# Kernel tuning notes

Measured on AMD Instinct MI355X. Metric: run time of the kernel, lower is better.

Reference implementation:

```python
import jax, jax.numpy as jnp
import numpy as np

E, H, I = 8, 1024, 512          # experts, hidden, moe_intermediate
NG, TKG, TOPK = 4, 2, 4          # n_group, topk_group, num_experts_per_tok
SCALE = 2.5                      # routed_scaling_factor


def _mlp(x, wg, wu, wd):
    # SwiGLU MLP: down(silu(gate(x)) * up(x)), all bias-free
    return (jax.nn.silu(x @ wg) * (x @ wu)) @ wd


def setup_inputs() -> dict:
    key = jax.random.key(0)
    ks = jax.random.split(key, 8)
    s = 0.02
    return {
        "hidden_states": jax.random.normal(ks[0], (32, 256, H), jnp.float32),
        "gate_w": jax.random.normal(ks[1], (E, H), jnp.float32) * np.float32(np.sqrt(2.0 / H)),
        "correction_bias": jnp.zeros((E,), jnp.float32),
        "Wg": jax.random.normal(ks[2], (E, H, I), jnp.float32) * s,
        "Wu": jax.random.normal(ks[3], (E, H, I), jnp.float32) * s,
        "Wd": jax.random.normal(ks[4], (E, I, H), jnp.float32) * s,
        "Wg_s": jax.random.normal(ks[5], (H, I), jnp.float32) * s,
        "Wu_s": jax.random.normal(ks[6], (H, I), jnp.float32) * s,
        "Wd_s": jax.random.normal(ks[7], (I, H), jnp.float32) * s,
    }


def reference(hidden_states, gate_w, correction_bias, Wg, Wu, Wd, Wg_s, Wu_s, Wd_s):
    B, T, _ = hidden_states.shape
    x = hidden_states.reshape(-1, H)                     # [N, H]
    N = x.shape[0]

    # ---- TopkRouter + route_tokens_to_experts (float32 router math) ----
    logits = x @ gate_w.T                                # [N, E]
    scores = jax.nn.sigmoid(logits)
    scores_c = scores + correction_bias                  # scores for choice
    grp = scores_c.reshape(N, NG, E // NG)
    group_scores = jnp.sum(jax.lax.top_k(grp, 2)[0], axis=-1)        # [N, NG]
    grp_idx = jax.lax.top_k(group_scores, TKG)[1]                    # [N, TKG]
    group_mask = jnp.zeros_like(group_scores).at[
        jnp.arange(N)[:, None], grp_idx].set(1.0)                    # [N, NG]
    score_mask = jnp.repeat(group_mask, E // NG, axis=-1) > 0.5      # [N, E]
    scores_for_choice = jnp.where(score_mask, scores_c, 0.0)
    topk_idx = jax.lax.top_k(scores_for_choice, TOPK)[1]             # [N, K]
    topk_w = jnp.take_along_axis(scores, topk_idx, axis=-1)          # [N, K]
    topk_w = topk_w / (jnp.sum(topk_w, axis=-1, keepdims=True) + 1e-20)
    topk_w = topk_w * SCALE

    # ---- DSNaiveMoE: equivalent dense-expert combine ----
    # combine weight per (token, expert); zero for unrouted pairs, so the
    # dense evaluation produces exactly the gather/scatter loop's result.
    cw = jnp.sum(jax.nn.one_hot(topk_idx, E, dtype=topk_w.dtype) * topk_w[..., None], axis=1)  # [N, E]
    g = jnp.einsum('nh,ehi->eni', x, Wg)
    u = jnp.einsum('nh,ehi->eni', x, Wu)
    y = jnp.einsum('eni,eih->enh', jax.nn.silu(g) * u, Wd)           # [E, N, H]
    routed = jnp.einsum('enh,ne->nh', y, cw)                          # [N, H]

    # ---- shared expert on residual input (replaces residual add) ----
    out = routed + _mlp(x, Wg_s, Wu_s, Wd_s)
    return out.reshape(B, T, H)
```

## Files before the change

### kernel.cpp

```cpp
#include <hip/hip_runtime.h>

#define E_ 8
#define H_ 1024
#define I_ 512
#define NE 9
#define NTOK 8192
#define NROWS 40960

typedef __bf16 bf16;
typedef __bf16 bf16x8 __attribute__((ext_vector_type(8)));
typedef __bf16 bf16x4 __attribute__((ext_vector_type(4)));
typedef float f32x4 __attribute__((ext_vector_type(4)));

__device__ __forceinline__ void gload16(const bf16* g, bf16* l) {
  __builtin_amdgcn_global_load_lds(
      (const __attribute__((address_space(1))) void*)g,
      (__attribute__((address_space(3))) void*)l,
      16, 0, 0);
}

#define PREP_CONV 2048
#define PREP_TRANS 3456
__global__ __launch_bounds__(256) void prep_kernel(
    const float* __restrict__ x, const float* __restrict__ gw,
    const float* __restrict__ bias,
    const float* __restrict__ Wg, const float* __restrict__ Wu,
    const float* __restrict__ Wd, const float* __restrict__ Wgs,
    const float* __restrict__ Wus, const float* __restrict__ Wds,
    bf16* __restrict__ xb, bf16* __restrict__ BgT, bf16* __restrict__ BuT,
    bf16* __restrict__ WdT, int4* __restrict__ topk_e, float4* __restrict__ topk_w) {
  __shared__ bf16 tile[64][66];
  int bid = blockIdx.x;
  int t = threadIdx.x;

  if (bid < PREP_CONV) {
    size_t base = (size_t)bid * 1024 + t;
#pragma unroll
    for (int j = 0; j < 4; j++) {
      f32x4 v = ((const f32x4*)x)[base + 256 * j];
      bf16x4 o = {(bf16)v.x, (bf16)v.y, (bf16)v.z, (bf16)v.w};
      ((bf16x4*)xb)[base + 256 * j] = o;
    }
    return;
  }
  if (bid < PREP_CONV + PREP_TRANS) {
    int b = bid - PREP_CONV;
    int job = b >> 7;
    int tl = b & 127;
    const float* src;
    bf16* dst;
    int C, dst_ld, tr, tc;
    if (job < 18) {
      int e = job % 9;
      if (job < 9) src = (e < 8) ? Wg + (size_t)e * H_ * I_ : Wgs;
      else         src = (e < 8) ? Wu + (size_t)e * H_ * I_ : Wus;
      dst = ((job < 9) ? BgT : BuT) + (size_t)e * I_ * H_;
      C = I_; dst_ld = H_;
      tr = tl >> 3; tc = tl & 7;
    } else {
      int e = job - 18;
      src = (e < 8) ? Wd + (size_t)e * I_ * H_ : Wds;
      dst = WdT + (size_t)e * H_ * I_;
      C = H_; dst_ld = I_;
      tr = tl >> 4; tc = tl & 15;
    }
    int lx = t & 63, ly = t >> 6;
#pragma unroll
    for (int j = 0; j < 16; j++) {
      int rl = j * 4 + ly;
      tile[lx][rl] = (bf16)src[(size_t)(tr * 64 + rl) * C + tc * 64 + lx];
    }
    __syncthreads();
#pragma unroll
    for (int j = 0; j < 16; j++) {
      int cl = j * 4 + ly;
      dst[(size_t)(tc * 64 + cl) * dst_ld + tr * 64 + lx] = tile[cl][lx];
    }
    return;
  }
  int rb = bid - PREP_CONV - PREP_TRANS;
  int l = t & 63, w = t >> 6;
  int n = rb * 4 + w;
  const f32x4* xr = (const f32x4*)(x + (size_t)n * H_ + l * 16);
  float xv[16];
#pragma unroll
  for (int q = 0; q < 4; q++) {
    f32x4 v = xr[q];
    xv[q * 4 + 0] = v.x; xv[q * 4 + 1] = v.y; xv[q * 4 + 2] = v.z; xv[q * 4 + 3] = v.w;
  }
  float acc[E_];
#pragma unroll
  for (int e = 0; e < E_; e++) {
    const f32x4* gr = (const f32x4*)(gw + e * H_ + l * 16);
    float a = 0.f;
#pragma unroll
    for (int q = 0; q < 4; q++) {
      f32x4 g = gr[q];
      a += xv[q * 4 + 0] * g.x + xv[q * 4 + 1] * g.y + xv[q * 4 + 2] * g.z + xv[q * 4 + 3] * g.w;
    }
    acc[e] = a;
  }
#pragma unroll
  for (int off = 32; off > 0; off >>= 1) {
    float tmp[E_];
#pragma unroll
    for (int e = 0; e < E_; e++) tmp[e] = __shfl_xor(acc[e], off, 64);
#pragma unroll
    for (int e = 0; e < E_; e++) acc[e] += tmp[e];
  }
  if (l == 0) {
    float s[E_], sc[E_];
#pragma unroll
    for (int e = 0; e < E_; e++) {
      s[e] = 1.f / (1.f + __expf(-acc[e]));
      sc[e] = s[e] + bias[e];
    }
    float gs[4];
#pragma unroll
    for (int g = 0; g < 4; g++) gs[g] = sc[2 * g] + sc[2 * g + 1];
    int g0 = 0;
    for (int g = 1; g < 4; g++) if (gs[g] > gs[g0]) g0 = g;
    int g1 = -1;
    for (int g = 0; g < 4; g++) {
      if (g == g0) continue;
      if (g1 < 0 || gs[g] > gs[g1]) g1 = g;
    }
    int es[4] = {2 * g0, 2 * g0 + 1, 2 * g1, 2 * g1 + 1};
    float wsum = 1e-20f;
    for (int j = 0; j < 4; j++) wsum += s[es[j]];
    float inv = 2.5f / wsum;
    topk_e[n] = (int4){es[0], es[1], es[2], es[3]};
    topk_w[n] = (float4){s[es[0]] * inv, s[es[1]] * inv, s[es[2]] * inv, s[es[3]] * inv};
  }
}

__global__ __launch_bounds__(256) void compact_kernel(
    const int4* __restrict__ topk_e, const float4* __restrict__ topk_w,
    int* __restrict__ cnt, int* __restrict__ idx, float* __restrict__ cwp,
    int* __restrict__ tokpos) {
  __shared__ int hist[E_];
  __shared__ int base[E_];
  int t = threadIdx.x;
  if (t < E_) hist[t] = 0;
  __syncthreads();
  int n = blockIdx.x * 256 + t;
  int4 e4 = topk_e[n];
  float4 w4 = topk_w[n];
  int le[4] = {e4.x, e4.y, e4.z, e4.w};
  float lw[4] = {w4.x, w4.y, w4.z, w4.w};
  int lpos[4];
#pragma unroll
  for (int j = 0; j < 4; j++) lpos[j] = atomicAdd(&hist[le[j]], 1);
  __syncthreads();
  if (t < E_) base[t] = atomicAdd(&cnt[t], hist[t]);
  __syncthreads();
#pragma unroll
  for (int j = 0; j < 4; j++) {
    int p = base[le[j]] + lpos[j];
    idx[le[j] * NTOK + p] = n;
    cwp[le[j] * NTOK + p] = lw[j];
    tokpos[n * 4 + j] = (le[j] << 13) | p;
  }
}

__device__ __forceinline__ bool slot_decode(const int* cnt, int slot,
                                            int& e, int& m0, int& ne, int& off_e) {
  int off = 0, s = slot;
  for (int ee = 0; ee < NE; ee++) {
    int c = (ee < E_) ? cnt[ee] : NTOK;
    int tl = (c + 127) >> 7;
    if (s < tl) { e = ee; m0 = s * 128; ne = c; off_e = off; return true; }
    s -= tl;
    off += c;
  }
  return false;
}


__global__ __launch_bounds__(256, 2) void gemm1_kernel(
    const bf16* __restrict__ X, const bf16* __restrict__ BgT,
    const bf16* __restrict__ BuT, const int* __restrict__ idx,
    const float* __restrict__ cwp, const int* __restrict__ cnt,
    bf16* __restrict__ Tc) {
  int e, m0, ne, off_e;
  if (!slot_decode(cnt, blockIdx.y, e, m0, ne, off_e)) return;

  __shared__ bf16 As[128 * 64], Bgs[128 * 64], Bus[128 * 64];
  int t = threadIdx.x;
  int l = t & 63, w = t >> 6;
  int wm = w >> 1, wn = w & 1;
  int n0 = blockIdx.x * 128;

  f32x4 accg[4][4], accu[4][4];
#pragma unroll
  for (int mi = 0; mi < 4; mi++)
#pragma unroll
    for (int ni = 0; ni < 4; ni++) {
      accg[mi][ni] = (f32x4){0.f, 0.f, 0.f, 0.f};
      accu[mi][ni] = (f32x4){0.f, 0.f, 0.f, 0.f};
    }

  int srow = t >> 3;
  int scol = (((t & 7) ^ ((t >> 3) & 7)) * 8);
  int rid[4];
#pragma unroll
  for (int i = 0; i < 4; i++) {
    int r = m0 + srow + 32 * i;
    rid[i] = (e < 8) ? ((r < ne) ? idx[e * NTOK + r] : 0) : r;
  }
  const bf16* gg = BgT + (size_t)e * I_ * H_ + (size_t)(n0 + srow) * H_ + scol;
  const bf16* gu = BuT + (size_t)e * I_ * H_ + (size_t)(n0 + srow) * H_ + scol;
  bf16* la = As + w * 512;
  bf16* lg = Bgs + w * 512;
  bf16* lu = Bus + w * 512;

  for (int k0 = 0; k0 < H_; k0 += 64) {
#pragma unroll
    for (int i = 0; i < 4; i++) {
      gload16(X + (size_t)rid[i] * H_ + scol + k0, la + i * 2048);
      gload16(gg + (size_t)i * 32 * H_ + k0, lg + i * 2048);
      gload16(gu + (size_t)i * 32 * H_ + k0, lu + i * 2048);
    }
    __syncthreads();
#pragma unroll
    for (int ks = 0; ks < 2; ks++) {
      int ko = (((ks * 4 + (l >> 4)) ^ (l & 7)) * 8);
      int ar = wm * 64 + (l & 15);
      int br = wn * 64 + (l & 15);
      bf16x8 af[4], bg[4], bu[4];
#pragma unroll
      for (int mi = 0; mi < 4; mi++)
        af[mi] = *(const bf16x8*)(As + (ar + mi * 16) * 64 + ko);
#pragma unroll
      for (int ni = 0; ni < 4; ni++) {
        bg[ni] = *(const bf16x8*)(Bgs + (br + ni * 16) * 64 + ko);
        bu[ni] = *(const bf16x8*)(Bus + (br + ni * 16) * 64 + ko);
      }
#pragma unroll
      for (int mi = 0; mi < 4; mi++)
#pragma unroll
        for (int ni = 0; ni < 4; ni++) {
          accg[mi][ni] = __builtin_amdgcn_mfma_f32_16x16x32_bf16(af[mi], bg[ni], accg[mi][ni], 0, 0, 0);
          accu[mi][ni] = __builtin_amdgcn_mfma_f32_16x16x32_bf16(af[mi], bu[ni], accu[mi][ni], 0, 0, 0);
        }
    }
    __syncthreads();
  }
#pragma unroll
  for (int mi = 0; mi < 4; mi++) {
#pragma unroll
    for (int r = 0; r < 4; r++) {
      int lr = wm * 64 + mi * 16 + (l >> 4) * 4 + r;
      int pr = m0 + lr;
      if (pr < ne) {
        float c = (e < 8) ? cwp[e * NTOK + pr] : 1.0f;
#pragma unroll
        for (int ni = 0; ni < 4; ni++) {
          float g = accg[mi][ni][r];
          float u = accu[mi][ni][r];
          float val = c * (g / (1.f + __expf(-g))) * u;
          int col = n0 + wn * 64 + ni * 16 + (l & 15);
          Tc[(size_t)(off_e + pr) * I_ + col] = (bf16)val;
        }
      }
    }
  }
}

__global__ __launch_bounds__(256, 3) void gemm2_kernel(
    const bf16* __restrict__ Tc, const bf16* __restrict__ WdT,
    const int* __restrict__ cnt, bf16* __restrict__ Yp) {
  int e, m0, ne, off_e;
  if (!slot_decode(cnt, blockIdx.y, e, m0, ne, off_e)) return;

  __shared__ bf16 As[128 * 64], Bs[128 * 64];
  int t = threadIdx.x;
  int l = t & 63, w = t >> 6;
  int wm = w >> 1, wn = w & 1;
  int n0 = blockIdx.x * 128;

  f32x4 acc[4][4];
#pragma unroll
  for (int mi = 0; mi < 4; mi++)
#pragma unroll
    for (int ni = 0; ni < 4; ni++) acc[mi][ni] = (f32x4){0.f, 0.f, 0.f, 0.f};

  int srow = t >> 3;
  int scol = (((t & 7) ^ ((t >> 3) & 7)) * 8);
  const bf16* ga = Tc + (size_t)(off_e + m0 + srow) * I_ + scol;
  const bf16* gb = WdT + (size_t)e * H_ * I_ + (size_t)(n0 + srow) * I_ + scol;
  bf16* la = As + w * 512;
  bf16* lb = Bs + w * 512;

  for (int k0 = 0; k0 < I_; k0 += 64) {
#pragma unroll
    for (int i = 0; i < 4; i++) {
      gload16(ga + (size_t)i * 32 * I_ + k0, la + i * 2048);
      gload16(gb + (size_t)i * 32 * I_ + k0, lb + i * 2048);
    }
    __syncthreads();
#pragma unroll
    for (int ks = 0; ks < 2; ks++) {
      int ko = (((ks * 4 + (l >> 4)) ^ (l & 7)) * 8);
      int ar = wm * 64 + (l & 15);
      int br = wn * 64 + (l & 15);
      bf16x8 af[4], bfv[4];
#pragma unroll
      for (int mi = 0; mi < 4; mi++)
        af[mi] = *(const bf16x8*)(As + (ar + mi * 16) * 64 + ko);
#pragma unroll
      for (int ni = 0; ni < 4; ni++)
        bfv[ni] = *(const bf16x8*)(Bs + (br + ni * 16) * 64 + ko);
#pragma unroll
      for (int mi = 0; mi < 4; mi++)
#pragma unroll
        for (int ni = 0; ni < 4; ni++)
          acc[mi][ni] = __builtin_amdgcn_mfma_f32_16x16x32_bf16(af[mi], bfv[ni], acc[mi][ni], 0, 0, 0);
    }
    __syncthreads();
  }
#pragma unroll
  for (int mi = 0; mi < 4; mi++) {
#pragma unroll
    for (int r = 0; r < 4; r++) {
      int lr = wm * 64 + mi * 16 + (l >> 4) * 4 + r;
      int pr = m0 + lr;
      if (pr < ne) {
#pragma unroll
        for (int ni = 0; ni < 4; ni++) {
          int col = n0 + wn * 64 + ni * 16 + (l & 15);
          Yp[(size_t)(off_e + pr) * H_ + col] = (bf16)acc[mi][ni][r];
        }
      }
    }
  }
}

__global__ __launch_bounds__(256) void combine_kernel(
    const int* __restrict__ cnt, const int* __restrict__ tokpos,
    const bf16* __restrict__ Yp, float* __restrict__ out) {
  int t = threadIdx.x;
  int tok = blockIdx.x * 2 + (t >> 7);
  int cb = (t & 127) * 8;
  int off[E_];
  int a = 0;
#pragma unroll
  for (int e = 0; e < E_; e++) { off[e] = a; a += cnt[e]; }
  float sum[8];
  {
    bf16x8 v = *(const bf16x8*)(Yp + (size_t)(32768 + tok) * H_ + cb);
#pragma unroll
    for (int q = 0; q < 8; q++) sum[q] = (float)v[q];
  }
#pragma unroll
  for (int j = 0; j < 4; j++) {
    int tp = tokpos[tok * 4 + j];
    int e = tp >> 13, p = tp & 8191;
    bf16x8 v = *(const bf16x8*)(Yp + (size_t)(off[e] + p) * H_ + cb);
#pragma unroll
    for (int q = 0; q < 8; q++) sum[q] += (float)v[q];
  }
  float* op = out + (size_t)tok * H_ + cb;
  *(f32x4*)(op) = (f32x4){sum[0], sum[1], sum[2], sum[3]};
  *(f32x4*)(op + 4) = (f32x4){sum[4], sum[5], sum[6], sum[7]};
}

extern "C" void kernel_launch(void* const* d_in, const int* in_sizes, int n_in,
                              void* d_out, int out_size, void* d_ws, size_t ws_size,
                              hipStream_t stream) {
  const float* x   = (const float*)d_in[0];
  const float* gw  = (const float*)d_in[1];
  const float* cb  = (const float*)d_in[2];
  const float* Wg  = (const float*)d_in[3];
  const float* Wu  = (const float*)d_in[4];
  const float* Wd  = (const float*)d_in[5];
  const float* Wgs = (const float*)d_in[6];
  const float* Wus = (const float*)d_in[7];
  const float* Wds = (const float*)d_in[8];

  char* ws = (char*)d_ws;
  size_t off = 0;
  int*    cnt    = (int*)(ws + off);    off += 64;
  int*    idx    = (int*)(ws + off);    off += (size_t)E_ * NTOK * 4;
  float*  cwp    = (float*)(ws + off);  off += (size_t)E_ * NTOK * 4;
  int4*   topk_e = (int4*)(ws + off);   off += (size_t)NTOK * 16;
  float4* topk_w = (float4*)(ws + off); off += (size_t)NTOK * 16;
  int*    tokpos = (int*)(ws + off);    off += (size_t)NTOK * 4 * 4;
  bf16* BgT = (bf16*)(ws + off);  off += (size_t)NE * I_ * H_ * 2;
  bf16* BuT = (bf16*)(ws + off);  off += (size_t)NE * I_ * H_ * 2;
  bf16* WdT = (bf16*)(ws + off);  off += (size_t)NE * H_ * I_ * 2;
  bf16* Xb  = (bf16*)(ws + off);  off += (size_t)NTOK * H_ * 2;
  bf16* Tc  = (bf16*)(ws + off);  off += (size_t)NROWS * I_ * 2;
  bf16* Yp  = (bf16*)(ws + off);  off += (size_t)NROWS * H_ * 2;

  hipMemsetAsync(cnt, 0, 64, stream);
  hipLaunchKernelGGL(prep_kernel, dim3(PREP_CONV + PREP_TRANS + NTOK / 4), dim3(256), 0, stream,
                     x, gw, cb, Wg, Wu, Wd, Wgs, Wus, Wds,
                     Xb, BgT, BuT, WdT, topk_e, topk_w);
  hipLaunchKernelGGL(compact_kernel, dim3(NTOK / 256), dim3(256), 0, stream,
                     topk_e, topk_w, cnt, idx, cwp, tokpos);
  hipLaunchKernelGGL(gemm1_kernel, dim3(4, 328), dim3(256), 0, stream,
                     Xb, BgT, BuT, idx, cwp, cnt, Tc);
  hipLaunchKernelGGL(gemm2_kernel, dim3(8, 328), dim3(256), 0, stream,
                     Tc, WdT, cnt, Yp);
  hipLaunchKernelGGL(combine_kernel, dim3(NTOK / 2), dim3(256), 0, stream,
                     cnt, tokpos, Yp, (float*)d_out);
}
```

Before: 379.4 us.

## Use persistent XCD-aware tile scheduling so each XCD handles one expert

After: 536.5 us. +41.4%, slower.

```diff
diff --git a/kernel.cpp b/kernel.cpp
--- a/kernel.cpp
+++ b/kernel.cpp
@@ -163,173 +163,187 @@
   }
 }
 
-__device__ __forceinline__ bool slot_decode(const int* cnt, int slot,
-                                            int& e, int& m0, int& ne, int& off_e) {
-  int off = 0, s = slot;
-  for (int ee = 0; ee < NE; ee++) {
-    int c = (ee < E_) ? cnt[ee] : NTOK;
-    int tl = (c + 127) >> 7;
-    if (s < tl) { e = ee; m0 = s * 128; ne = c; off_e = off; return true; }
-    s -= tl;
-    off += c;
+__device__ __forceinline__ bool xcd_decode(const int* cnt, int g, int j, int ntiles,
+                                           int& e, int& m0, int& ne, int& off_e, int& n0) {
+  int ne_g = cnt[g];
+  int Tg = ((ne_g + 127) >> 7) * ntiles;
+  if (j < Tg) {
+    e = g; ne = ne_g;
+    m0 = (j / ntiles) * 128; n0 = (j % ntiles) * 128;
+    int off = 0;
+    for (int ee = 0; ee < E_; ee++) off += (ee < g) ? cnt[ee] : 0;
+    off_e = off;
+    return true;
+  }
+  int s = (j - Tg) * 8 + g;
+  if (s < 64 * ntiles) {
+    e = 8; ne = NTOK; off_e = 4 * NTOK;
+    m0 = (s / ntiles) * 128; n0 = (s % ntiles) * 128;
+    return true;
   }
   return false;
 }
 
 
-__global__ __launch_bounds__(256, 2) void gemm1_kernel(
+__global__ __launch_bounds__(256, 3) void gemm1_kernel(
     const bf16* __restrict__ X, const bf16* __restrict__ BgT,
     const bf16* __restrict__ BuT, const int* __restrict__ idx,
     const float* __restrict__ cwp, const int* __restrict__ cnt,
     bf16* __restrict__ Tc) {
-  int e, m0, ne, off_e;
-  if (!slot_decode(cnt, blockIdx.y, e, m0, ne, off_e)) return;
-
   __shared__ bf16 As[128 * 64], Bgs[128 * 64], Bus[128 * 64];
   int t = threadIdx.x;
   int l = t & 63, w = t >> 6;
   int wm = w >> 1, wn = w & 1;
-  int n0 = blockIdx.x * 128;
-
-  f32x4 accg[4][4], accu[4][4];
-#pragma unroll
-  for (int mi = 0; mi < 4; mi++)
-#pragma unroll
-    for (int ni = 0; ni < 4; ni++) {
-      accg[mi][ni] = (f32x4){0.f, 0.f, 0.f, 0.f};
-      accu[mi][ni] = (f32x4){0.f, 0.f, 0.f, 0.f};
-    }
-
   int srow = t >> 3;
   int scol = (((t & 7) ^ ((t >> 3) & 7)) * 8);
-  int rid[4];
-#pragma unroll
-  for (int i = 0; i < 4; i++) {
-    int r = m0 + srow + 32 * i;
-    rid[i] = (e < 8) ? ((r < ne) ? idx[e * NTOK + r] : 0) : r;
-  }
-  const bf16* gg = BgT + (size_t)e * I_ * H_ + (size_t)(n0 + srow) * H_ + scol;
-  const bf16* gu = BuT + (size_t)e * I_ * H_ + (size_t)(n0 + srow) * H_ + scol;
   bf16* la = As + w * 512;
   bf16* lg = Bgs + w * 512;
   bf16* lu = Bus + w * 512;
-
-  for (int k0 = 0; k0 < H_; k0 += 64) {
+  int g = blockIdx.x & 7;
+  int S = gridDim.x >> 3;
+
+  for (int j = blockIdx.x >> 3; ; j += S) {
+    int e, m0, ne, off_e, n0;
+    if (!xcd_decode(cnt, g, j, 4, e, m0, ne, off_e, n0)) break;
+
+    f32x4 accg[4][4], accu[4][4];
+#pragma unroll
+    for (int mi = 0; mi < 4; mi++)
+#pragma unroll
+      for (int ni = 0; ni < 4; ni++) {
+        accg[mi][ni] = (f32x4){0.f, 0.f, 0.f, 0.f};
+        accu[mi][ni] = (f32x4){0.f, 0.f, 0.f, 0.f};
+      }
+
+    int rid[4];
 #pragma unroll
     for (int i = 0; i < 4; i++) {
-      gload16(X + (size_t)rid[i] * H_ + scol + k0, la + i * 2048);
-      gload16(gg + (size_t)i * 32 * H_ + k0, lg + i * 2048);
-      gload16(gu + (size_t)i * 32 * H_ + k0, lu + i * 2048);
-    }
-    __syncthreads();
-#pragma unroll
-    for (int ks = 0; ks < 2; ks++) {
-      int ko = (((ks * 4 + (l >> 4)) ^ (l & 7)) * 8);
-      int ar = wm * 64 + (l & 15);
-      int br = wn * 64 + (l & 15);
-      bf16x8 af[4], bg[4], bu[4];
-#pragma unroll
-      for (int mi = 0; mi < 4; mi++)
-        af[mi] = *(const bf16x8*)(As + (ar + mi * 16) * 64 + ko);
-#pragma unroll
-      for (int ni = 0; ni < 4; ni++) {
-        bg[ni] = *(const bf16x8*)(Bgs + (br + ni * 16) * 64 + ko);
-        bu[ni] = *(const bf16x8*)(Bus + (br + ni * 16) * 64 + ko);
-      }
-#pragma unroll
-      for (int mi = 0; mi < 4; mi++)
+      int r = m0 + srow + 32 * i;
+      rid[i] = (e < 8) ? ((r < ne) ? idx[e * NTOK + r] : 0) : r;
+    }
+    const bf16* gg = BgT + (size_t)e * I_ * H_ + (size_t)(n0 + srow) * H_ + scol;
+    const bf16* gu = BuT + (size_t)e * I_ * H_ + (size_t)(n0 + srow) * H_ + scol;
+
+    for (int k0 = 0; k0 < H_; k0 += 64) {
+#pragma unroll
+      for (int i = 0; i < 4; i++) {
+        gload16(X + (size_t)rid[i] * H_ + scol + k0, la + i * 2048);
+        gload16(gg + (size_t)i * 32 * H_ + k0, lg + i * 2048);
+        gload16(gu + (size_t)i * 32 * H_ + k0, lu + i * 2048);
+      }
+      __syncthreads();
+#pragma unroll
+      for (int ks = 0; ks < 2; ks++) {
+        int ko = (((ks * 4 + (l >> 4)) ^ (l & 7)) * 8);
+        int ar = wm * 64 + (l & 15);
+        int br = wn * 64 + (l & 15);
+        bf16x8 af[4], bg[4], bu[4];
+#pragma unroll
+        for (int mi = 0; mi < 4; mi++)
+          af[mi] = *(const bf16x8*)(As + (ar + mi * 16) * 64 + ko);
 #pragma unroll
         for (int ni = 0; ni < 4; ni++) {
-          accg[mi][ni] = __builtin_amdgcn_mfma_f32_16x16x32_bf16(af[mi], bg[ni], accg[mi][ni], 0, 0, 0);
-          accu[mi][ni] = __builtin_amdgcn_mfma_f32_16x16x32_bf16(af[mi], bu[ni], accu[mi][ni], 0, 0, 0);
+          bg[ni] = *(const bf16x8*)(Bgs + (br + ni * 16) * 64 + ko);
+          bu[ni] = *(const bf16x8*)(Bus + (br + ni * 16) * 64 + ko);
         }
-    }
-    __syncthreads();
-  }
-#pragma unroll
-  for (int mi = 0; mi < 4; mi++) {
-#pragma unroll
-    for (int r = 0; r < 4; r++) {
-      int lr = wm * 64 + mi * 16 + (l >> 4) * 4 + r;
-      int pr = m0 + lr;
-      if (pr < ne) {
-        float c = (e < 8) ? cwp[e * NTOK + pr] : 1.0f;
-#pragma unroll
-        for (int ni = 0; ni < 4; ni++) {
-          float g = accg[mi][ni][r];
-          float u = accu[mi][ni][r];
-          float val = c * (g / (1.f + __expf(-g))) * u;
-          int col = n0 + wn * 64 + ni * 16 + (l & 15);
-          Tc[(size_t)(off_e + pr) * I_ + col] = (bf16)val;
+#pragma unroll
+        for (int mi = 0; mi < 4; mi++)
+#pragma unroll
+          for (int ni = 0; ni < 4; ni++) {
+            accg[mi][ni] = __builtin_amdgcn_mfma_f32_16x16x32_bf16(af[mi], bg[ni], accg[mi][ni], 0, 0, 0);
+            accu[mi][ni] = __builtin_amdgcn_mfma_f32_16x16x32_bf16(af[mi], bu[ni], accu[mi][ni], 0, 0, 0);
+          }
+      }
+      __syncthreads();
+    }
+#pragma unroll
+    for (int mi = 0; mi < 4; mi++) {
+#pragma unroll
+      for (int r = 0; r < 4; r++) {
+        int lr = wm * 64 + mi * 16 + (l >> 4) * 4 + r;
+        int pr = m0 + lr;
+        if (pr < ne) {
+          float c = (e < 8) ? cwp[e * NTOK + pr] : 1.0f;
+#pragma unroll
+          for (int ni = 0; ni < 4; ni++) {
+            float gv = accg[mi][ni][r];
+            float uv = accu[mi][ni][r];
+            float val = c * (gv / (1.f + __expf(-gv))) * uv;
+            int col = n0 + wn * 64 + ni * 16 + (l & 15);
+            Tc[(size_t)(off_e + pr) * I_ + col] = (bf16)val;
+          }
         }
       }
     }
   }
 }
 
-__global__ __launch_bounds__(256, 3) void gemm2_kernel(
+__global__ __launch_bounds__(256, 4) void gemm2_kernel(
     const bf16* __restrict__ Tc, const bf16* __restrict__ WdT,
     const int* __restrict__ cnt, bf16* __restrict__ Yp) {
-  int e, m0, ne, off_e;
-  if (!slot_decode(cnt, blockIdx.y, e, m0, ne, off_e)) return;
-
   __shared__ bf16 As[128 * 64], Bs[128 * 64];
   int t = threadIdx.x;
   int l = t & 63, w = t >> 6;
   int wm = w >> 1, wn = w & 1;
-  int n0 = blockIdx.x * 128;
-
-  f32x4 acc[4][4];
-#pragma unroll
-  for (int mi = 0; mi < 4; mi++)
-#pragma unroll
-    for (int ni = 0; ni < 4; ni++) acc[mi][ni] = (f32x4){0.f, 0.f, 0.f, 0.f};
-
   int srow = t >> 3;
   int scol = (((t & 7) ^ ((t >> 3) & 7)) * 8);
-  const bf16* ga = Tc + (size_t)(off_e + m0 + srow) * I_ + scol;
-  const bf16* gb = WdT + (size_t)e * H_ * I_ + (size_t)(n0 + srow) * I_ + scol;
   bf16* la = As + w * 512;
   bf16* lb = Bs + w * 512;
-
-  for (int k0 = 0; k0 < I_; k0 += 64) {
-#pragma unroll
-    for (int i = 0; i < 4; i++) {
-      gload16(ga + (size_t)i * 32 * I_ + k0, la + i * 2048);
-      gload16(gb + (size_t)i * 32 * I_ + k0, lb + i * 2048);
-    }
-    __syncthreads();
-#pragma unroll
-    for (int ks = 0; ks < 2; ks++) {
-      int ko = (((ks * 4 + (l >> 4)) ^ (l & 7)) * 8);
-      int ar = wm * 64 + (l & 15);
-      int br = wn * 64 + (l & 15);
-      bf16x8 af[4], bfv[4];
-#pragma unroll
-      for (int mi = 0; mi < 4; mi++)
-        af[mi] = *(const bf16x8*)(As + (ar + mi * 16) * 64 + ko);
-#pragma unroll
-      for (int ni = 0; ni < 4; ni++)
-        bfv[ni] = *(const bf16x8*)(Bs + (br + ni * 16) * 64 + ko);
-#pragma unroll
-      for (int mi = 0; mi < 4; mi++)
+  int g = blockIdx.x & 7;
+  int S = gridDim.x >> 3;
+
+  for (int j = blockIdx.x >> 3; ; j += S) {
+    int e, m0, ne, off_e, n0;
+    if (!xcd_decode(cnt, g, j, 8, e, m0, ne, off_e, n0)) break;
+
+    f32x4 acc[4][4];
+#pragma unroll
+    for (int mi = 0; mi < 4; mi++)
+#pragma unroll
+      for (int ni = 0; ni < 4; ni++) acc[mi][ni] = (f32x4){0.f, 0.f, 0.f, 0.f};
+
+    const bf16* ga = Tc + (size_t)(off_e + m0 + srow) * I_ + scol;
+    const bf16* gb = WdT + (size_t)e * H_ * I_ + (size_t)(n0 + srow) * I_ + scol;
+
+    for (int k0 = 0; k0 < I_; k0 += 64) {
+#pragma unroll
+      for (int i = 0; i < 4; i++) {
+        gload16(ga + (size_t)i * 32 * I_ + k0, la + i * 2048);
+        gload16(gb + (size_t)i * 32 * I_ + k0, lb + i * 2048);
+      }
+      __syncthreads();
+#pragma unroll
+      for (int ks = 0; ks < 2; ks++) {
+        int ko = (((ks * 4 + (l >> 4)) ^ (l & 7)) * 8);
+        int ar = wm * 64 + (l & 15);
+        int br = wn * 64 + (l & 15);
+        bf16x8 af[4], bfv[4];
+#pragma unroll
+        for (int mi = 0; mi < 4; mi++)
+          af[mi] = *(const bf16x8*)(As + (ar + mi * 16) * 64 + ko);
 #pragma unroll
         for (int ni = 0; ni < 4; ni++)
-          acc[mi][ni] = __builtin_amdgcn_mfma_f32_16x16x32_bf16(af[mi], bfv[ni], acc[mi][ni], 0, 0, 0);
-    }
-    __syncthreads();
-  }
-#pragma unroll
-  for (int mi = 0; mi < 4; mi++) {
-#pragma unroll
-    for (int r = 0; r < 4; r++) {
-      int lr = wm * 64 + mi * 16 + (l >> 4) * 4 + r;
-      int pr = m0 + lr;
-      if (pr < ne) {
-#pragma unroll
-        for (int ni = 0; ni < 4; ni++) {
-          int col = n0 + wn * 64 + ni * 16 + (l & 15);
-          Yp[(size_t)(off_e + pr) * H_ + col] = (bf16)acc[mi][ni][r];
+          bfv[ni] = *(const bf16x8*)(Bs + (br + ni * 16) * 64 + ko);
+#pragma unroll
+        for (int mi = 0; mi < 4; mi++)
+#pragma unroll
+          for (int ni = 0; ni < 4; ni++)
+            acc[mi][ni] = __builtin_amdgcn_mfma_f32_16x16x32_bf16(af[mi], bfv[ni], acc[mi][ni], 0, 0, 0);
+      }
+      __syncthreads();
+    }
+#pragma unroll
+    for (int mi = 0; mi < 4; mi++) {
+#pragma unroll
+      for (int r = 0; r < 4; r++) {
+        int lr = wm * 64 + mi * 16 + (l >> 4) * 4 + r;
+        int pr = m0 + lr;
+        if (pr < ne) {
+#pragma unroll
+          for (int ni = 0; ni < 4; ni++) {
+            int col = n0 + wn * 64 + ni * 16 + (l & 15);
+            Yp[(size_t)(off_e + pr) * H_ + col] = (bf16)acc[mi][ni][r];
+          }
         }
       }
     }
@@ -399,9 +413,9 @@
                      Xb, BgT, BuT, WdT, topk_e, topk_w);
   hipLaunchKernelGGL(compact_kernel, dim3(NTOK / 256), dim3(256), 0, stream,
                      topk_e, topk_w, cnt, idx, cwp, tokpos);
-  hipLaunchKernelGGL(gemm1_kernel, dim3(4, 328), dim3(256), 0, stream,
+  hipLaunchKernelGGL(gemm1_kernel, dim3(8 * 160), dim3(256), 0, stream,
                      Xb, BgT, BuT, idx, cwp, cnt, Tc);
-  hipLaunchKernelGGL(gemm2_kernel, dim3(8, 328), dim3(256), 0, stream,
+  hipLaunchKernelGGL(gemm2_kernel, dim3(8 * 320), dim3(256), 0, stream,
                      Tc, WdT, cnt, Yp);
   hipLaunchKernelGGL(combine_kernel, dim3(NTOK / 2), dim3(256), 0, stream,
                      cnt, tokpos, Yp, (float*)d_out);
```
